# Kernel optimization log

Measured on AMD Instinct MI355X. Metric: run time of the kernel, lower is better.

Reference implementation:

```python
import jax, jax.numpy as jnp
import numpy as np

B, N, C = 2, 2048, 768
H = 12
HD = C // H  # 64


def setup_inputs() -> dict:
    key = jax.random.key(0)
    ks = jax.random.split(key, 6)
    s = 0.02
    x = jax.random.normal(ks[0], (B, N, C), dtype=jnp.float32)
    xpos = jnp.arange(B * N, dtype=jnp.int64).reshape(B, N) % N
    W_qkv = jax.random.normal(ks[1], (3 * C, C), dtype=jnp.float32) * s
    b_qkv = jnp.zeros((3 * C,), dtype=jnp.float32)
    W_proj = jax.random.normal(ks[2], (C, C), dtype=jnp.float32) * s
    b_proj = jnp.zeros((C,), dtype=jnp.float32)
    return {"x": x, "xpos": xpos, "W_qkv": W_qkv, "b_qkv": b_qkv,
            "W_proj": W_proj, "b_proj": b_proj}


def reference(x, xpos, W_qkv, b_qkv, W_proj, b_proj):
    # rope is None in this configuration -> xpos is unused, matching torch module.
    Bx, Nx, Cx = x.shape
    scale = (Cx // H) ** -0.5
    qkv = x @ W_qkv.T + b_qkv                     # [B, N, 3C]
    qkv = qkv.reshape(Bx, Nx, 3, H, HD)
    q = jnp.einsum('bnhd->bhnd', qkv[:, :, 0])    # [B, H, N, HD]
    k = jnp.einsum('bnhd->bhnd', qkv[:, :, 1])
    v = jnp.einsum('bnhd->bhnd', qkv[:, :, 2])
    attn = jnp.einsum('bhnd,bhmd->bhnm', q, k) * scale  # [B, H, N, N]
    attn = jax.nn.softmax(attn, axis=-1)
    out = jnp.einsum('bhnm,bhmd->bhnd', attn, v)  # [B, H, N, HD]
    out = jnp.einsum('bhnd->bnhd', out).reshape(Bx, Nx, Cx)
    return out @ W_proj.T + b_proj
```

## Files before the change

kernel.cpp:

```cpp
#include <hip/hip_runtime.h>
#include <hip/hip_bf16.h>


typedef _Float16 half8 __attribute__((ext_vector_type(8)));
typedef _Float16 half4_t __attribute__((ext_vector_type(4)));
typedef float floatx4 __attribute__((ext_vector_type(4)));

#define LDA 72
#define LDP 72
#define SCALE_LOG2E 0.1803368801111204f

constexpr int XH_OFF    = 0;
constexpr int WQKV_OFF  = XH_OFF + 4096 * 768;
constexpr int WPROJ_OFF = WQKV_OFF + 2304 * 768;
constexpr int QK_OFF    = WPROJ_OFF + 768 * 768;
constexpr int VTH_OFF   = QK_OFF + 4096 * 1536;
constexpr int PO_OFF    = VTH_OFF + 24 * 64 * 2048;
constexpr int PSTAT_OFF = PO_OFF + 2 * 24 * 2048 * 64;

__device__ __forceinline__ void gl16(const _Float16* g, _Float16* l) {
  __builtin_amdgcn_global_load_lds(
      (const __attribute__((address_space(1))) unsigned int*)g,
      (__attribute__((address_space(3))) unsigned int*)l, 16, 0, 0);
}

__global__ __launch_bounds__(256) void cvt_all(const float* __restrict__ x,
                                               const float* __restrict__ wqkv,
                                               const float* __restrict__ wproj,
                                               _Float16* __restrict__ ws) {
  constexpr int n1 = 4096 * 768 / 4;
  constexpr int n2 = 2304 * 768 / 4;
  int i = blockIdx.x * 256 + threadIdx.x;
  const float* src; _Float16* dst; int j;
  if (i < n1)           { src = x;     dst = ws + XH_OFF;    j = i; }
  else if (i < n1 + n2) { src = wqkv;  dst = ws + WQKV_OFF;  j = i - n1; }
  else                  { src = wproj; dst = ws + WPROJ_OFF; j = i - n1 - n2; }
  floatx4 f = *(const floatx4*)(src + 4 * j);
  half4_t h;
  h[0] = (_Float16)f[0]; h[1] = (_Float16)f[1];
  h[2] = (_Float16)f[2]; h[3] = (_Float16)f[3];
  *(half4_t*)(dst + 4 * j) = h;
}

__global__ __launch_bounds__(256) void qkv_gemm(const _Float16* __restrict__ xh,
                                                const _Float16* __restrict__ wh,
                                                const float* __restrict__ bias,
                                                _Float16* __restrict__ qkh,
                                                _Float16* __restrict__ vth) {
  __shared__ __align__(16) _Float16 sA[64 * 64];
  __shared__ __align__(16) _Float16 sB[128 * 64];
  const int tid = threadIdx.x;
  const int nblk = blockIdx.x % 18, mblk = blockIdx.x / 18;
  const int lane = tid & 63, w = tid >> 6;
  const int lane15 = lane & 15, quad = lane >> 4;
  const int lrow = lane >> 3, lchunk = lane & 7;

  floatx4 acc[4][2];
#pragma unroll
  for (int mt = 0; mt < 4; ++mt)
#pragma unroll
    for (int nt = 0; nt < 2; ++nt) acc[mt][nt] = (floatx4){0.f, 0.f, 0.f, 0.f};

  for (int kt = 0; kt < 12; ++kt) {
    if (kt) __syncthreads();
#pragma unroll
    for (int i = 0; i < 6; ++i) {
      int g = w * 48 + 8 * i;
      if (g < 64)
        gl16(xh + (mblk * 64 + g + lrow) * 768 + kt * 64 + lchunk * 8, sA + g * 64);
      else
        gl16(wh + (nblk * 128 + (g - 64) + lrow) * 768 + kt * 64 + lchunk * 8,
             sB + (g - 64) * 64);
    }
    __syncthreads();
#pragma unroll
    for (int ks = 0; ks < 2; ++ks) {
      half8 af[4], bf[2];
#pragma unroll
      for (int mt = 0; mt < 4; ++mt)
        af[mt] = *(const half8*)(sA + (mt * 16 + lane15) * 64 + ks * 32 + quad * 8);
#pragma unroll
      for (int nt = 0; nt < 2; ++nt)
        bf[nt] = *(const half8*)(sB + (w * 32 + nt * 16 + lane15) * 64 + ks * 32 + quad * 8);
#pragma unroll
      for (int mt = 0; mt < 4; ++mt)
#pragma unroll
        for (int nt = 0; nt < 2; ++nt)
          acc[mt][nt] = __builtin_amdgcn_mfma_f32_16x16x32_f16(af[mt], bf[nt], acc[mt][nt], 0, 0, 0);
    }
  }

  const int mbase = mblk * 64;
#pragma unroll
  for (int nt = 0; nt < 2; ++nt) {
    int cbase = nblk * 128 + w * 32 + nt * 16;
    float bv = bias[cbase + lane15];
    if (cbase < 1536) {
      int col = cbase + lane15;
      float sc = (cbase < 768) ? SCALE_LOG2E : 1.0f;
#pragma unroll
      for (int mt = 0; mt < 4; ++mt)
#pragma unroll
        for (int r = 0; r < 4; ++r) {
          int token = mbase + mt * 16 + quad * 4 + r;
          qkh[token * 1536 + col] = (_Float16)((acc[mt][nt][r] + bv) * sc);
        }
    } else {
      int dcol = cbase - 1536 + lane15;
      int h = dcol >> 6, d = dcol & 63;
#pragma unroll
      for (int mt = 0; mt < 4; ++mt) {
        int tok0 = mbase + mt * 16 + quad * 4;
        int b = tok0 >> 11, n0 = tok0 & 2047;
        int bh = b * 12 + h;
        half4_t hv;
#pragma unroll
        for (int r = 0; r < 4; ++r) hv[r] = (_Float16)(acc[mt][nt][r] + bv);
        *(half4_t*)(vth + (bh * 64 + d) * 2048 + n0) = hv;
      }
    }
  }
}

__global__ __launch_bounds__(512) void attn_fused(const _Float16* __restrict__ qkh,
                                                  const _Float16* __restrict__ vth,
                                                  _Float16* __restrict__ pO,
                                                  float* __restrict__ pL) {
  __shared__ __align__(16) _Float16 sK[64 * LDA];
  __shared__ __align__(16) _Float16 sVT[64 * LDA];
  __shared__ __align__(16) _Float16 sP[8 * 16 * LDP];
  const int tid = threadIdx.x;
  const int bx = blockIdx.x;
  const int bh = bx % 24;
  const int rest = bx / 24;
  const int ks = rest & 1, qt = rest >> 1;
  const int b = bh / 12, h = bh % 12;
  const int lane = tid & 63, w = tid >> 6;
  const int lane15 = lane & 15, quad = lane >> 4;
  const int chunk = tid & 7, rbase = tid >> 3;
  const int wq = w >> 2, ww = w & 3;
  _Float16* sPw = sP + w * 16 * LDP;

  const int qkbase = b * 2048 * 1536 + h * 64;
  const int qrow = qt * 128 + wq * 64 + ww * 16 + lane15;
  half8 qa0 = *(const half8*)(qkh + qkbase + qrow * 1536 + quad * 8);
  half8 qa1 = *(const half8*)(qkh + qkbase + qrow * 1536 + 32 + quad * 8);

  const int kt0 = ks * 16;
  const _Float16* kp = qkh + qkbase + 768 + (kt0 * 64 + rbase) * 1536 + chunk * 8;
  const _Float16* vp = vth + bh * 64 * 2048 + rbase * 2048 + kt0 * 64 + chunk * 8;

  floatx4 O[4];
#pragma unroll
  for (int dt = 0; dt < 4; ++dt) O[dt] = (floatx4){0.f, 0.f, 0.f, 0.f};
  float lrow = 0.f;

  for (int kt = 0; kt < 16; ++kt) {
    half8 tk = *(const half8*)kp;
    half8 tv = *(const half8*)vp;
    kp += 64 * 1536;
    vp += 64;
    if (kt) __syncthreads();
    *(half8*)(sK + rbase * LDA + chunk * 8) = tk;
    *(half8*)(sVT + rbase * LDA + chunk * 8) = tv;
    __syncthreads();

    floatx4 s[4];
#pragma unroll
    for (int nt = 0; nt < 4; ++nt) {
      half8 kf0 = *(const half8*)(sK + (nt * 16 + lane15) * LDA + quad * 8);
      half8 kf1 = *(const half8*)(sK + (nt * 16 + lane15) * LDA + 32 + quad * 8);
      floatx4 a = (floatx4){0.f, 0.f, 0.f, 0.f};
      a = __builtin_amdgcn_mfma_f32_16x16x32_f16(kf0, qa0, a, 0, 0, 0);
      a = __builtin_amdgcn_mfma_f32_16x16x32_f16(kf1, qa1, a, 0, 0, 0);
      s[nt] = a;
    }

    float rsum = 0.f;
#pragma unroll
    for (int nt = 0; nt < 4; ++nt)
#pragma unroll
      for (int r = 0; r < 4; ++r) {
        float p = exp2f(fminf(s[nt][r], 30.f));
        s[nt][r] = p;
        rsum += p;
      }
    rsum += __shfl_xor(rsum, 16, 64);
    rsum += __shfl_xor(rsum, 32, 64);
    lrow += rsum;

#pragma unroll
    for (int nt = 0; nt < 4; ++nt) {
      half4_t hp;
#pragma unroll
      for (int r = 0; r < 4; ++r) hp[r] = (_Float16)s[nt][r];
      *(half4_t*)(sPw + lane15 * LDP + nt * 16 + quad * 4) = hp;
    }
    asm volatile("s_waitcnt lgkmcnt(0)" ::: "memory");

#pragma unroll
    for (int kk = 0; kk < 2; ++kk) {
      half8 pa = *(const half8*)(sPw + lane15 * LDP + kk * 32 + quad * 8);
#pragma unroll
      for (int dt = 0; dt < 4; ++dt) {
        half8 vb = *(const half8*)(sVT + (dt * 16 + lane15) * LDA + kk * 32 + quad * 8);
        O[dt] = __builtin_amdgcn_mfma_f32_16x16x32_f16(pa, vb, O[dt], 0, 0, 0);
      }
    }
  }

  const int prow = (ks * 24 + bh) * 2048 + qt * 128 + wq * 64 + ww * 16;
#pragma unroll
  for (int dt = 0; dt < 4; ++dt)
#pragma unroll
    for (int r = 0; r < 4; ++r)
      pO[(prow + quad * 4 + r) * 64 + dt * 16 + lane15] = (_Float16)O[dt][r];
  if (lane < 16) pL[prow + lane] = lrow;
}

__global__ __launch_bounds__(256) void proj_gemm(const _Float16* __restrict__ pO,
                                                 const float* __restrict__ pL,
                                                 const _Float16* __restrict__ wh,
                                                 const float* __restrict__ bias,
                                                 float* __restrict__ out) {
  __shared__ __align__(16) _Float16 sA[64 * 72];
  __shared__ __align__(16) _Float16 sB[128 * 64];
  const int tid = threadIdx.x;
  const int nblk = blockIdx.x % 6, mblk = blockIdx.x / 6;
  const int lane = tid & 63, w = tid >> 6;
  const int lane15 = lane & 15, quad = lane >> 4;
  const int lrow = lane >> 3, lchunk = lane & 7;
  const int arow = tid >> 2, achk = tid & 3;
  const int tok0 = mblk * 64;
  const int b = tok0 >> 11, tokl = tok0 & 2047;

  floatx4 acc[4][2];
#pragma unroll
  for (int mt = 0; mt < 4; ++mt)
#pragma unroll
    for (int nt = 0; nt < 2; ++nt) acc[mt][nt] = (floatx4){0.f, 0.f, 0.f, 0.f};

  for (int kt = 0; kt < 12; ++kt) {
    const int bh = b * 12 + kt;
    const int row1 = bh * 2048 + tokl + arow;
    const int row2 = (24 + bh) * 2048 + tokl + arow;
    float f = 1.0f / (pL[row1] + pL[row2]);

    if (kt) __syncthreads();
#pragma unroll
    for (int i = 0; i < 4; ++i) {
      int g = w * 32 + 8 * i;
      gl16(wh + (nblk * 128 + g + lrow) * 768 + kt * 64 + lchunk * 8, sB + g * 64);
    }
#pragma unroll
    for (int cc = 0; cc < 2; ++cc) {
      int c8 = achk + 4 * cc;
      half8 o1 = *(const half8*)(pO + row1 * 64 + c8 * 8);
      half8 o2 = *(const half8*)(pO + row2 * 64 + c8 * 8);
      half8 o;
#pragma unroll
      for (int e = 0; e < 8; ++e)
        o[e] = (_Float16)(f * ((float)o1[e] + (float)o2[e]));
      *(half8*)(sA + arow * 72 + c8 * 8) = o;
    }
    __syncthreads();

#pragma unroll
    for (int ksplit = 0; ksplit < 2; ++ksplit) {
      half8 af[4], bf[2];
#pragma unroll
      for (int mt = 0; mt < 4; ++mt)
        af[mt] = *(const half8*)(sA + (mt * 16 + lane15) * 72 + ksplit * 32 + quad * 8);
#pragma unroll
      for (int nt = 0; nt < 2; ++nt)
        bf[nt] = *(const half8*)(sB + (w * 32 + nt * 16 + lane15) * 64 + ksplit * 32 + quad * 8);
#pragma unroll
      for (int mt = 0; mt < 4; ++mt)
#pragma unroll
        for (int nt = 0; nt < 2; ++nt)
          acc[mt][nt] = __builtin_amdgcn_mfma_f32_16x16x32_f16(af[mt], bf[nt], acc[mt][nt], 0, 0, 0);
    }
  }

  const int mbase = mblk * 64;
#pragma unroll
  for (int nt = 0; nt < 2; ++nt) {
    int col = nblk * 128 + w * 32 + nt * 16 + lane15;
    float bv = bias[col];
#pragma unroll
    for (int mt = 0; mt < 4; ++mt)
#pragma unroll
      for (int r = 0; r < 4; ++r) {
        int token = mbase + mt * 16 + quad * 4 + r;
        out[token * 768 + col] = acc[mt][nt][r] + bv;
      }
  }
}

extern "C" void kernel_launch(void* const* d_in, const int* in_sizes, int n_in,
                              void* d_out, int out_size, void* d_ws, size_t ws_size,
                              hipStream_t stream) {
  const float* x     = (const float*)d_in[0];
  const float* wqkv  = (const float*)d_in[2];
  const float* bqkv  = (const float*)d_in[3];
  const float* wproj = (const float*)d_in[4];
  const float* bproj = (const float*)d_in[5];
  float* out = (float*)d_out;

  _Float16* ws = (_Float16*)d_ws;
  _Float16* xh     = ws + XH_OFF;
  _Float16* wqkvh  = ws + WQKV_OFF;
  _Float16* wprojh = ws + WPROJ_OFF;
  _Float16* qkh    = ws + QK_OFF;
  _Float16* vth    = ws + VTH_OFF;
  _Float16* pO     = ws + PO_OFF;
  float*    pL     = (float*)(ws + PSTAT_OFF);

  constexpr int total_v4 = (4096 * 768 + 2304 * 768 + 768 * 768) / 4;
  cvt_all<<<total_v4 / 256, 256, 0, stream>>>(x, wqkv, wproj, ws);
  qkv_gemm<<<64 * 18, 256, 0, stream>>>(xh, wqkvh, bqkv, qkh, vth);
  attn_fused<<<24 * 32, 512, 0, stream>>>(qkh, vth, pO, pL);
  proj_gemm<<<64 * 6, 256, 0, stream>>>(pO, pL, wprojh, bproj, out);
}
```

Before: 180.1 us.

## Rewrite attention kernel with 32x32 MFMA, register P, double-buffered swizzled LDS

Restructures the fused attention kernel to use 32x32x16 MFMA tiles, with four waves each owning 32 query rows instead of eight waves owning 16 rows. The P tile is passed from the QK product to the PV product in registers via permlane32_swap, removing the LDS round trip. K/V tiles are double-buffered in XOR-swizzled LDS with register prefetch, so there is one barrier per iteration and padding is no longer needed. This cuts LDS traffic and sync overhead, at the cost of higher register pressure and fewer threads per block.

```diff
diff --git a/kernel.cpp b/kernel.cpp
--- a/kernel.cpp
+++ b/kernel.cpp
@@ -5,9 +5,10 @@
 typedef _Float16 half8 __attribute__((ext_vector_type(8)));
 typedef _Float16 half4_t __attribute__((ext_vector_type(4)));
 typedef float floatx4 __attribute__((ext_vector_type(4)));
-
-#define LDA 72
-#define LDP 72
+typedef float floatx16 __attribute__((ext_vector_type(16)));
+typedef unsigned int uintx4 __attribute__((ext_vector_type(4)));
+typedef unsigned int uintx2 __attribute__((ext_vector_type(2)));
+
 #define SCALE_LOG2E 0.1803368801111204f
 
 constexpr int XH_OFF    = 0;
@@ -122,13 +123,12 @@
   }
 }
 
-__global__ __launch_bounds__(512) void attn_fused(const _Float16* __restrict__ qkh,
-                                                  const _Float16* __restrict__ vth,
-                                                  _Float16* __restrict__ pO,
-                                                  float* __restrict__ pL) {
-  __shared__ __align__(16) _Float16 sK[64 * LDA];
-  __shared__ __align__(16) _Float16 sVT[64 * LDA];
-  __shared__ __align__(16) _Float16 sP[8 * 16 * LDP];
+__global__ __launch_bounds__(256, 3) void attn_fused(const _Float16* __restrict__ qkh,
+                                                     const _Float16* __restrict__ vth,
+                                                     _Float16* __restrict__ pO,
+                                                     float* __restrict__ pL) {
+  __shared__ __align__(16) _Float16 sK[2][64 * 64];
+  __shared__ __align__(16) _Float16 sVT[2][64 * 64];
   const int tid = threadIdx.x;
   const int bx = blockIdx.x;
   const int bh = bx % 24;
@@ -136,86 +136,126 @@
   const int ks = rest & 1, qt = rest >> 1;
   const int b = bh / 12, h = bh % 12;
   const int lane = tid & 63, w = tid >> 6;
-  const int lane15 = lane & 15, quad = lane >> 4;
-  const int chunk = tid & 7, rbase = tid >> 3;
-  const int wq = w >> 2, ww = w & 3;
-  _Float16* sPw = sP + w * 16 * LDP;
+  const int q = lane & 31, hi = lane >> 5;
 
   const int qkbase = b * 2048 * 1536 + h * 64;
-  const int qrow = qt * 128 + wq * 64 + ww * 16 + lane15;
-  half8 qa0 = *(const half8*)(qkh + qkbase + qrow * 1536 + quad * 8);
-  half8 qa1 = *(const half8*)(qkh + qkbase + qrow * 1536 + 32 + quad * 8);
-
-  const int kt0 = ks * 16;
-  const _Float16* kp = qkh + qkbase + 768 + (kt0 * 64 + rbase) * 1536 + chunk * 8;
-  const _Float16* vp = vth + bh * 64 * 2048 + rbase * 2048 + kt0 * 64 + chunk * 8;
-
-  floatx4 O[4];
-#pragma unroll
-  for (int dt = 0; dt < 4; ++dt) O[dt] = (floatx4){0.f, 0.f, 0.f, 0.f};
+  const int qrow = qt * 128 + w * 32 + q;
+
+  half8 qf[4];
+#pragma unroll
+  for (int c = 0; c < 4; ++c)
+    qf[c] = *(const half8*)(qkh + qkbase + qrow * 1536 + c * 16 + hi * 8);
+
+  const int srow = tid >> 2, sc = tid & 3;
+  const int key0 = ks * 1024;
+  const _Float16* kp = qkh + qkbase + 768 + (key0 + srow) * 1536 + sc * 8;
+  const _Float16* vp = vth + (bh * 64 + srow) * 2048 + key0 + sc * 8;
+  const int sw0 = srow * 64 + ((sc ^ (srow & 7)) * 8);
+  const int sw1 = srow * 64 + (((sc + 4) ^ (srow & 7)) * 8);
+
+  floatx16 O[2];
+#pragma unroll
+  for (int dg = 0; dg < 2; ++dg)
+#pragma unroll
+    for (int i = 0; i < 16; ++i) O[dg][i] = 0.f;
   float lrow = 0.f;
 
+  half8 rk0 = *(const half8*)kp, rk1 = *(const half8*)(kp + 32);
+  half8 rv0 = *(const half8*)vp, rv1 = *(const half8*)(vp + 32);
+  kp += 64 * 1536; vp += 64;
+  { _Float16* nK = &sK[0][0]; _Float16* nV = &sVT[0][0];
+    *(half8*)(nK + sw0) = rk0; *(half8*)(nK + sw1) = rk1;
+    *(half8*)(nV + sw0) = rv0; *(half8*)(nV + sw1) = rv1; }
+  rk0 = *(const half8*)kp; rk1 = *(const half8*)(kp + 32);
+  rv0 = *(const half8*)vp; rv1 = *(const half8*)(vp + 32);
+  kp += 64 * 1536; vp += 64;
+
   for (int kt = 0; kt < 16; ++kt) {
-    half8 tk = *(const half8*)kp;
-    half8 tv = *(const half8*)vp;
-    kp += 64 * 1536;
-    vp += 64;
-    if (kt) __syncthreads();
-    *(half8*)(sK + rbase * LDA + chunk * 8) = tk;
-    *(half8*)(sVT + rbase * LDA + chunk * 8) = tv;
     __syncthreads();
-
-    floatx4 s[4];
-#pragma unroll
-    for (int nt = 0; nt < 4; ++nt) {
-      half8 kf0 = *(const half8*)(sK + (nt * 16 + lane15) * LDA + quad * 8);
-      half8 kf1 = *(const half8*)(sK + (nt * 16 + lane15) * LDA + 32 + quad * 8);
-      floatx4 a = (floatx4){0.f, 0.f, 0.f, 0.f};
-      a = __builtin_amdgcn_mfma_f32_16x16x32_f16(kf0, qa0, a, 0, 0, 0);
-      a = __builtin_amdgcn_mfma_f32_16x16x32_f16(kf1, qa1, a, 0, 0, 0);
-      s[nt] = a;
-    }
-
+    const _Float16* cK = &sK[kt & 1][0];
+    const _Float16* cV = &sVT[kt & 1][0];
+    if (kt < 15) {
+      _Float16* nK = &sK[(kt + 1) & 1][0];
+      _Float16* nV = &sVT[(kt + 1) & 1][0];
+      *(half8*)(nK + sw0) = rk0; *(half8*)(nK + sw1) = rk1;
+      *(half8*)(nV + sw0) = rv0; *(half8*)(nV + sw1) = rv1;
+      if (kt < 14) {
+        rk0 = *(const half8*)kp; rk1 = *(const half8*)(kp + 32);
+        rv0 = *(const half8*)vp; rv1 = *(const half8*)(vp + 32);
+        kp += 64 * 1536; vp += 64;
+      }
+    }
+
+    floatx16 s[2];
+#pragma unroll
+    for (int og = 0; og < 2; ++og)
+#pragma unroll
+      for (int i = 0; i < 16; ++i) s[og][i] = 0.f;
+#pragma unroll
+    for (int c = 0; c < 4; ++c) {
+      const int rc = c * 2 + hi;
+#pragma unroll
+      for (int og = 0; og < 2; ++og) {
+        const int krow = og * 32 + q;
+        half8 kf = *(const half8*)(cK + krow * 64 + ((rc ^ (krow & 7)) * 8));
+        s[og] = __builtin_amdgcn_mfma_f32_32x32x16_f16(kf, qf[c], s[og], 0, 0, 0);
+      }
+    }
+
+    float p[2][16];
     float rsum = 0.f;
 #pragma unroll
-    for (int nt = 0; nt < 4; ++nt)
-#pragma unroll
-      for (int r = 0; r < 4; ++r) {
-        float p = exp2f(fminf(s[nt][r], 30.f));
-        s[nt][r] = p;
-        rsum += p;
-      }
-    rsum += __shfl_xor(rsum, 16, 64);
-    rsum += __shfl_xor(rsum, 32, 64);
+    for (int og = 0; og < 2; ++og)
+#pragma unroll
+      for (int r = 0; r < 16; ++r) {
+        float e = exp2f(fminf(s[og][r], 30.f));
+        p[og][r] = e;
+        rsum += e;
+      }
     lrow += rsum;
 
-#pragma unroll
-    for (int nt = 0; nt < 4; ++nt) {
-      half4_t hp;
-#pragma unroll
-      for (int r = 0; r < 4; ++r) hp[r] = (_Float16)s[nt][r];
-      *(half4_t*)(sPw + lane15 * LDP + nt * 16 + quad * 4) = hp;
-    }
-    asm volatile("s_waitcnt lgkmcnt(0)" ::: "memory");
-
-#pragma unroll
-    for (int kk = 0; kk < 2; ++kk) {
-      half8 pa = *(const half8*)(sPw + lane15 * LDP + kk * 32 + quad * 8);
-#pragma unroll
-      for (int dt = 0; dt < 4; ++dt) {
-        half8 vb = *(const half8*)(sVT + (dt * 16 + lane15) * LDA + kk * 32 + quad * 8);
-        O[dt] = __builtin_amdgcn_mfma_f32_16x16x32_f16(pa, vb, O[dt], 0, 0, 0);
-      }
-    }
-  }
-
-  const int prow = (ks * 24 + bh) * 2048 + qt * 128 + wq * 64 + ww * 16;
-#pragma unroll
-  for (int dt = 0; dt < 4; ++dt)
-#pragma unroll
-    for (int r = 0; r < 4; ++r)
-      pO[(prow + quad * 4 + r) * 64 + dt * 16 + lane15] = (_Float16)O[dt][r];
-  if (lane < 16) pL[prow + lane] = lrow;
+    half8 bfrag[4];
+#pragma unroll
+    for (int m = 0; m < 4; ++m) {
+      const int og = m >> 1, rb = (m & 1) * 8;
+      unsigned ua = __builtin_bit_cast(unsigned,
+          __builtin_amdgcn_cvt_pkrtz(p[og][rb + 0], p[og][rb + 1]));
+      unsigned ub = __builtin_bit_cast(unsigned,
+          __builtin_amdgcn_cvt_pkrtz(p[og][rb + 2], p[og][rb + 3]));
+      unsigned uc = __builtin_bit_cast(unsigned,
+          __builtin_amdgcn_cvt_pkrtz(p[og][rb + 4], p[og][rb + 5]));
+      unsigned ud = __builtin_bit_cast(unsigned,
+          __builtin_amdgcn_cvt_pkrtz(p[og][rb + 6], p[og][rb + 7]));
+      uintx2 sAC = __builtin_amdgcn_permlane32_swap(ua, uc, false, false);
+      uintx2 sBD = __builtin_amdgcn_permlane32_swap(ub, ud, false, false);
+      uintx4 u; u[0] = sAC[0]; u[1] = sBD[0]; u[2] = sAC[1]; u[3] = sBD[1];
+      bfrag[m] = __builtin_bit_cast(half8, u);
+    }
+
+#pragma unroll
+    for (int m = 0; m < 4; ++m) {
+      const int rc2 = m * 2 + hi;
+#pragma unroll
+      for (int dg = 0; dg < 2; ++dg) {
+        const int vrow = dg * 32 + q;
+        half8 vf = *(const half8*)(cV + vrow * 64 + ((rc2 ^ (vrow & 7)) * 8));
+        O[dg] = __builtin_amdgcn_mfma_f32_32x32x16_f16(vf, bfrag[m], O[dg], 0, 0, 0);
+      }
+    }
+  }
+
+  const int prow = (ks * 24 + bh) * 2048 + qt * 128 + w * 32;
+#pragma unroll
+  for (int dg = 0; dg < 2; ++dg)
+#pragma unroll
+    for (int g2 = 0; g2 < 4; ++g2) {
+      half4_t hv;
+#pragma unroll
+      for (int e = 0; e < 4; ++e) hv[e] = (_Float16)O[dg][g2 * 4 + e];
+      *(half4_t*)(pO + (prow + q) * 64 + dg * 32 + g2 * 8 + hi * 4) = hv;
+    }
+  lrow += __shfl_xor(lrow, 32, 64);
+  if (lane < 32) pL[prow + lane] = lrow;
 }
 
 __global__ __launch_bounds__(256) void proj_gemm(const _Float16* __restrict__ pO,
@@ -319,6 +359,6 @@
   constexpr int total_v4 = (4096 * 768 + 2304 * 768 + 768 * 768) / 4;
   cvt_all<<<total_v4 / 256, 256, 0, stream>>>(x, wqkv, wproj, ws);
   qkv_gemm<<<64 * 18, 256, 0, stream>>>(xh, wqkvh, bqkv, qkh, vth);
-  attn_fused<<<24 * 32, 512, 0, stream>>>(qkh, vth, pO, pL);
+  attn_fused<<<24 * 32, 256, 0, stream>>>(qkh, vth, pO, pL);
   proj_gemm<<<64 * 6, 256, 0, stream>>>(pO, pL, wprojh, bproj, out);
 }
```

Result: no change. 183.0 us (+1.6%).
